# Optimization experiments

Hardware: AMD Instinct MI355X
Metric: run time of the kernel (lower is better)

The kernel has to match this reference:

```python
import jax, jax.numpy as jnp
import numpy as np

B, T, S, D, V = 8, 64, 512, 512, 50000


def setup_inputs() -> dict:
    key = jax.random.key(0)
    k1, k2, k3, k4, k5 = jax.random.split(key, 5)
    x = jax.random.normal(k1, (B, T, D), dtype=jnp.float32)
    attn_dist = jax.random.normal(k2, (B, T, S), dtype=jnp.float32)
    enc_batch_extend_vocab = jax.random.randint(k3, (B, S), 0, V, dtype=jnp.int64)
    W_proj = jax.random.normal(k4, (D, V), dtype=jnp.float32) * (1.0 / np.sqrt(D))
    b_proj = jnp.zeros((V,), dtype=jnp.float32)
    W_pgen = jax.random.normal(k5, (D, 1), dtype=jnp.float32) * (1.0 / np.sqrt(D))
    b_pgen = jnp.zeros((1,), dtype=jnp.float32)
    return {"x": x, "attn_dist": attn_dist,
            "enc_batch_extend_vocab": enc_batch_extend_vocab,
            "W_proj": W_proj, "b_proj": b_proj,
            "W_pgen": W_pgen, "b_pgen": b_pgen}


def reference(x, attn_dist, enc_batch_extend_vocab, W_proj, b_proj, W_pgen, b_pgen):
    # pointer-generator head, temp=1, beam_search=False
    temp = 1.0
    # p_gen gate: [B, T, 1]
    alpha = jax.nn.sigmoid(jnp.einsum('btd,de->bte', x, W_pgen) + b_pgen)
    # vocab projection + softmax: [B, T, V]
    logit = jnp.einsum('btd,dv->btv', x, W_proj) + b_proj
    vocab_dist = jax.nn.softmax(logit / temp, axis=2)
    vocab_dist_ = alpha * vocab_dist
    # copy distribution over source positions: [B, T, S]
    attn = jax.nn.softmax(attn_dist / temp, axis=-1)
    attn_ = (1.0 - alpha) * attn
    # scatter_add copy probs into vocab dim (index broadcast over T)
    b_idx = jnp.arange(B)[:, None, None]        # [B,1,1]
    t_idx = jnp.arange(T)[None, :, None]        # [1,T,1]
    v_idx = enc_batch_extend_vocab[:, None, :]  # [B,1,S]
    merged = vocab_dist_.at[b_idx, t_idx, v_idx].add(attn_)
    return jnp.log(merged)
```

## Files before the change

### kernel.cpp

```cpp
#include <hip/hip_runtime.h>
#include <math.h>
#include <stdint.h>

#define B_ 8
#define T_ 64
#define S_ 512
#define D_ 512
#define V_ 50000
#define VP_ 50176
#define M_ (B_*T_)
#define ROWB_ ((size_t)V_ * 4)

typedef __bf16 bf16_t;
typedef bf16_t bf16x8 __attribute__((ext_vector_type(8)));
typedef float  f32x4  __attribute__((ext_vector_type(4)));

__device__ inline float blk_sum(float v, float* sm) {
    #pragma unroll
    for (int o = 32; o > 0; o >>= 1) v += __shfl_down(v, o);
    int lane = threadIdx.x & 63, wid = threadIdx.x >> 6;
    __syncthreads();
    if (lane == 0) sm[wid] = v;
    __syncthreads();
    return sm[0] + sm[1] + sm[2] + sm[3];
}

__device__ inline float blk_max(float v, float* sm) {
    #pragma unroll
    for (int o = 32; o > 0; o >>= 1) v = fmaxf(v, __shfl_down(v, o));
    int lane = threadIdx.x & 63, wid = threadIdx.x >> 6;
    __syncthreads();
    if (lane == 0) sm[wid] = v;
    __syncthreads();
    return fmaxf(fmaxf(sm[0], sm[1]), fmaxf(sm[2], sm[3]));
}

__device__ inline void unpack8(uint4 u, float f[8]) {
    uint32_t w0 = u.x, w1 = u.y, w2 = u.z, w3 = u.w;
    f[0] = __uint_as_float(w0 << 16); f[1] = __uint_as_float(w0 & 0xffff0000u);
    f[2] = __uint_as_float(w1 << 16); f[3] = __uint_as_float(w1 & 0xffff0000u);
    f[4] = __uint_as_float(w2 << 16); f[5] = __uint_as_float(w2 & 0xffff0000u);
    f[6] = __uint_as_float(w3 << 16); f[7] = __uint_as_float(w3 & 0xffff0000u);
}

#define CONVB_ (98 * 16)
#define LTP2_ 516

__global__ __launch_bounds__(256) void kprep(
    const float* __restrict__ W, bf16_t* __restrict__ Wt,
    const float* __restrict__ x, const float* __restrict__ attn_dist,
    const float* __restrict__ W_pgen, const float* __restrict__ b_pgen,
    float* __restrict__ logalpha_out, float* __restrict__ attn_out, bf16_t* __restrict__ xb,
    const int* __restrict__ idx, int* __restrict__ owner_g)
{
    __shared__ bf16_t lt[32 * LTP2_];
    int bid = blockIdx.x;
    int tid = threadIdx.x;

    if (bid < CONVB_) {
        int vt = bid >> 4;
        int kb = bid & 15;
        int v0 = vt * 512, k0 = kb * 32;

        #pragma unroll
        for (int p = 0; p < 16; p++) {
            int i = p * 256 + tid;
            int k = i >> 7;
            int c4 = i & 127;
            int v = c4 * 4;
            float4 val = make_float4(0.f, 0.f, 0.f, 0.f);
            if (v0 + v < V_)
                val = *reinterpret_cast<const float4*>(&W[(size_t)(k0 + k) * V_ + v0 + v]);
            union { bf16_t h[4]; uint2 u; } pk;
            pk.h[0] = (bf16_t)val.x; pk.h[1] = (bf16_t)val.y;
            pk.h[2] = (bf16_t)val.z; pk.h[3] = (bf16_t)val.w;
            *reinterpret_cast<uint2*>(&lt[k * LTP2_ + v]) = pk.u;
        }
        __syncthreads();

        #pragma unroll
        for (int p = 0; p < 8; p++) {
            int i = p * 256 + tid;
            int v = i >> 2;
            int q = i & 3;
            union { ushort h[8]; uint4 u; } pk;
            #pragma unroll
            for (int j = 0; j < 8; j++)
                pk.h[j] = *reinterpret_cast<const ushort*>(&lt[(q * 8 + j) * LTP2_ + v]);
            *reinterpret_cast<uint4*>(&Wt[(size_t)(v0 + v) * D_ + k0 + q * 8]) = pk.u;
        }
    } else if (bid < CONVB_ + M_) {
        float* sm = reinterpret_cast<float*>(lt);
        int row = bid - CONVB_;

        float2 xv = reinterpret_cast<const float2*>(x + (size_t)row * D_)[tid];
        float2 wv = reinterpret_cast<const float2*>(W_pgen)[tid];
        union { bf16_t h[2]; uint32_t u; } pk;
        pk.h[0] = (bf16_t)xv.x; pk.h[1] = (bf16_t)xv.y;
        reinterpret_cast<uint32_t*>(xb + (size_t)row * D_)[tid] = pk.u;

        float dot = blk_sum(xv.x * wv.x + xv.y * wv.y, sm);
        float alpha = 1.f / (1.f + expf(-(dot + b_pgen[0])));
        if (tid == 0) logalpha_out[row] = logf(alpha);

        float a0 = attn_dist[(size_t)row * S_ + tid];
        float a1 = attn_dist[(size_t)row * S_ + tid + 256];
        float mx = blk_max(fmaxf(a0, a1), sm);
        float e0 = expf(a0 - mx), e1 = expf(a1 - mx);
        float s = blk_sum(e0 + e1, sm);
        float scale = (1.f - alpha) / s;
        attn_out[(size_t)row * S_ + tid]       = e0 * scale;
        attn_out[(size_t)row * S_ + tid + 256] = e1 * scale;
    } else {
        int* ids = reinterpret_cast<int*>(lt);
        int b = bid - (CONVB_ + M_);
        for (int s = tid; s < S_; s += 256) ids[s] = idx[b * S_ + s];
        __syncthreads();
        for (int s = tid; s < S_; s += 256) {
            int v = ids[s], o = s;
            for (int s2 = 0; s2 < s; s2++) if (ids[s2] == v) { o = s2; break; }
            owner_g[b * S_ + s] = o;
        }
    }
}

#define GBM 128
#define GBN 128
#define GBK 32
#define NT2_ (D_/GBK)

__global__ __launch_bounds__(256) void k2_mfma(
    const bf16_t* __restrict__ A, const bf16_t* __restrict__ Wt,
    const float* __restrict__ bias, char* __restrict__ outB)
{
    __shared__ bf16_t As0[GBM][GBK], As1[GBM][GBK];
    __shared__ bf16_t Bs0[GBN][GBK], Bs1[GBN][GBK];
    int tid  = threadIdx.x;
    int lane = tid & 63;
    int w    = tid >> 6;
    int wm   = w >> 1, wn = w & 1;
    int bn = blockIdx.x * GBN;
    int bm = blockIdx.y * GBM;

    f32x4 acc[4][4] = {};

#define STAGE(dstA, dstB, k0)                                                          \
    {                                                                                  \
        _Pragma("unroll")                                                              \
        for (int i = 0; i < 2; i++) {                                                  \
            int e = (w * 2 + i) * 512 + lane * 8;                                      \
            int r = e >> 5, c = e & 31;                                                \
            __builtin_amdgcn_global_load_lds(                                          \
                (const __attribute__((address_space(1))) void*)                        \
                    &A[(size_t)(bm + r) * D_ + (k0) + c],                              \
                (__attribute__((address_space(3))) void*)&dstA[(w * 2 + i) * 16][0],   \
                16, 0, 0);                                                             \
            __builtin_amdgcn_global_load_lds(                                          \
                (const __attribute__((address_space(1))) void*)                        \
                    &Wt[(size_t)(bn + r) * D_ + (k0) + c],                             \
                (__attribute__((address_space(3))) void*)&dstB[(w * 2 + i) * 16][0],   \
                16, 0, 0);                                                             \
        }                                                                              \
    }

#define COMPUTE(srcA, srcB)                                                            \
    {                                                                                  \
        bf16x8 af[4], bfr[4];                                                          \
        int kb = (lane >> 4) * 8;                                                      \
        _Pragma("unroll")                                                              \
        for (int mi = 0; mi < 4; mi++)                                                 \
            af[mi] = *reinterpret_cast<const bf16x8*>(&srcA[wm * 64 + mi * 16 + (lane & 15)][kb]); \
        _Pragma("unroll")                                                              \
        for (int ni = 0; ni < 4; ni++)                                                 \
            bfr[ni] = *reinterpret_cast<const bf16x8*>(&srcB[wn * 64 + ni * 16 + (lane & 15)][kb]); \
        _Pragma("unroll")                                                              \
        for (int mi = 0; mi < 4; mi++)                                                 \
            _Pragma("unroll")                                                          \
            for (int ni = 0; ni < 4; ni++)                                             \
                acc[mi][ni] = __builtin_amdgcn_mfma_f32_16x16x32_bf16(af[mi], bfr[ni], acc[mi][ni], 0, 0, 0); \
    }

    STAGE(As0, Bs0, 0);
    asm volatile("s_waitcnt vmcnt(0)" ::: "memory");
    __syncthreads();

    #pragma unroll
    for (int tt = 0; tt < NT2_ / 2; tt++) {
        int k0 = tt * 2 * GBK;
        if (k0 + GBK < D_) STAGE(As1, Bs1, k0 + GBK);
        COMPUTE(As0, Bs0);
        asm volatile("s_waitcnt vmcnt(0)" ::: "memory");
        __syncthreads();
        if (k0 + 2 * GBK < D_) STAGE(As0, Bs0, k0 + 2 * GBK);
        COMPUTE(As1, Bs1);
        asm volatile("s_waitcnt vmcnt(0)" ::: "memory");
        __syncthreads();
    }
#undef STAGE
#undef COMPUTE

    int cm = bm + wm * 64, cn = bn + wn * 64;
    #pragma unroll
    for (int ni = 0; ni < 4; ni++) {
        int n = cn + ni * 16 + (lane & 15);
        float bv = (n < V_) ? bias[n] : 0.f;
        #pragma unroll
        for (int mi = 0; mi < 4; mi++) {
            int rbase = cm + mi * 16 + (lane >> 4) * 4;
            #pragma unroll
            for (int r = 0; r < 4; r++) {
                bf16_t val = (bf16_t)(acc[mi][ni][r] + bv);
                *reinterpret_cast<bf16_t*>(outB + (size_t)(rbase + r) * ROWB_ + 2 * (size_t)n) = val;
            }
        }
    }
}

#define CHUNK_ 2048
#define NCH_ ((V_ + CHUNK_ - 1) / CHUNK_)

__global__ __launch_bounds__(256) void k345_final(
    char* __restrict__ outB, const float* __restrict__ attn_, const int* __restrict__ idx,
    const int* __restrict__ owner_g, const float* __restrict__ logalpha)
{
    __shared__ float att[S_];
    __shared__ int own[S_], ids[S_];
    __shared__ float smm[4], sms[4];
    int row = blockIdx.x;
    int b = row >> 6;
    int tid = threadIdx.x;
    int lane = tid & 63, wid = tid >> 6;

    for (int s = tid; s < S_; s += 256) {
        att[s] = attn_[(size_t)row * S_ + s];
        own[s] = owner_g[b * S_ + s];
        ids[s] = idx[b * S_ + s];
    }

    const uint4* L4 = reinterpret_cast<const uint4*>(outB + (size_t)row * ROWB_);
    float m = -INFINITY, se = 0.f;
    for (int i = tid; i < V_ / 8; i += 256) {
        uint4 u = L4[i];
        float f[8]; unpack8(u, f);
        float m8 = fmaxf(fmaxf(fmaxf(f[0], f[1]), fmaxf(f[2], f[3])),
                         fmaxf(fmaxf(f[4], f[5]), fmaxf(f[6], f[7])));
        float mn = fmaxf(m, m8);
        se = se * __expf(m - mn)
           + __expf(f[0] - mn) + __expf(f[1] - mn) + __expf(f[2] - mn) + __expf(f[3] - mn)
           + __expf(f[4] - mn) + __expf(f[5] - mn) + __expf(f[6] - mn) + __expf(f[7] - mn);
        m = mn;
    }
    #pragma unroll
    for (int o = 32; o > 0; o >>= 1) {
        float m2 = __shfl_down(m, o);
        float s2 = __shfl_down(se, o);
        float mn = fmaxf(m, m2);
        if (mn == -INFINITY) { se = 0.f; }
        else se = se * __expf(m - mn) + s2 * __expf(m2 - mn);
        m = mn;
    }
    __syncthreads();
    if (lane == 0) { smm[wid] = m; sms[wid] = se; }
    __syncthreads();
    float M = smm[0], Ssum = sms[0];
    #pragma unroll
    for (int wv = 1; wv < 4; wv++) {
        float m2 = smm[wv], s2 = sms[wv];
        float mn = fmaxf(M, m2);
        if (mn != -INFINITY) Ssum = Ssum * __expf(M - mn) + s2 * __expf(m2 - mn);
        M = mn;
    }
    float logden = M + logf(Ssum);
    float c_ = logalpha[row] - logden;

    for (int s = tid; s < S_; s += 256)
        if (own[s] != s) atomicAdd(&att[own[s]], att[s]);
    __syncthreads();

    const ushort* Lrow = reinterpret_cast<const ushort*>(outB + (size_t)row * ROWB_);
    float* frow = reinterpret_cast<float*>(outB + (size_t)row * ROWB_);
    for (int c = NCH_ - 1; c >= 0; c--) {
        int i0 = c * CHUNK_ + tid * 8;
        uint4 u = make_uint4(0, 0, 0, 0);
        bool act = (i0 + 8 <= V_);
        if (act) u = *reinterpret_cast<const uint4*>(Lrow + i0);
        __syncthreads();
        if (act) {
            float f[8]; unpack8(u, f);
            float4 lo = make_float4(f[0] + c_, f[1] + c_, f[2] + c_, f[3] + c_);
            float4 hi = make_float4(f[4] + c_, f[5] + c_, f[6] + c_, f[7] + c_);
            *reinterpret_cast<float4*>(frow + i0)     = lo;
            *reinterpret_cast<float4*>(frow + i0 + 4) = hi;
        }
        __syncthreads();
    }

    for (int s = tid; s < S_; s += 256) {
        if (own[s] == s) {
            int v = ids[s];
            frow[v] = logf(expf(frow[v]) + att[s]);
        }
    }
}

__global__ __launch_bounds__(256) void k1_alpha_attn(
    const float* __restrict__ x, const float* __restrict__ attn_dist,
    const float* __restrict__ W_pgen, const float* __restrict__ b_pgen,
    float* __restrict__ logalpha_out, float* __restrict__ attn_out)
{
    __shared__ float sm[4];
    int row = blockIdx.x;
    int tid = threadIdx.x;
    float2 xv = reinterpret_cast<const float2*>(x + (size_t)row * D_)[tid];
    float2 wv = reinterpret_cast<const float2*>(W_pgen)[tid];
    float dot = blk_sum(xv.x * wv.x + xv.y * wv.y, sm);
    float alpha = 1.f / (1.f + expf(-(dot + b_pgen[0])));
    if (tid == 0) logalpha_out[row] = logf(alpha);
    float a0 = attn_dist[(size_t)row * S_ + tid];
    float a1 = attn_dist[(size_t)row * S_ + tid + 256];
    float mx = blk_max(fmaxf(a0, a1), sm);
    float e0 = expf(a0 - mx), e1 = expf(a1 - mx);
    float s = blk_sum(e0 + e1, sm);
    float scale = (1.f - alpha) / s;
    attn_out[(size_t)row * S_ + tid]       = e0 * scale;
    attn_out[(size_t)row * S_ + tid + 256] = e1 * scale;
}

__global__ __launch_bounds__(512) void k5a_owner(const int* __restrict__ idx, int* __restrict__ owner_g)
{
    __shared__ int ids[S_];
    int b = blockIdx.x;
    int s = threadIdx.x;
    ids[s] = idx[b * S_ + s];
    __syncthreads();
    int v = ids[s], o = s;
    for (int s2 = 0; s2 < s; s2++) if (ids[s2] == v) { o = s2; break; }
    owner_g[b * S_ + s] = o;
}

#define BM 64
#define BN 64
#define BK 16
__global__ __launch_bounds__(256) void k2_gemm(
    const float* __restrict__ A, const float* __restrict__ W,
    const float* __restrict__ bias, float* __restrict__ C)
{
    __shared__ float As2[BK][BM + 1];
    __shared__ float Bs2[BK][BN + 1];
    int bn = blockIdx.x * BN;
    int bm = blockIdx.y * BM;
    int tid = threadIdx.x;
    int tx = tid & 15;
    int ty = tid >> 4;
    bool full_n = (bn + BN <= V_);
    float acc[4][4] = {};
    for (int k0 = 0; k0 < D_; k0 += BK) {
        {
            int i = tid * 4;
            int row = i >> 4, col = i & 15;
            const float4 av = *reinterpret_cast<const float4*>(&A[(size_t)(bm + row) * D_ + k0 + col]);
            As2[col + 0][row] = av.x; As2[col + 1][row] = av.y;
            As2[col + 2][row] = av.z; As2[col + 3][row] = av.w;
        }
        {
            int i = tid * 4;
            int row = i >> 6, col = i & 63;
            int gn = bn + col;
            if (full_n) {
                const float4 bv = *reinterpret_cast<const float4*>(&W[(size_t)(k0 + row) * V_ + gn]);
                Bs2[row][col + 0] = bv.x; Bs2[row][col + 1] = bv.y;
                Bs2[row][col + 2] = bv.z; Bs2[row][col + 3] = bv.w;
            } else {
                #pragma unroll
                for (int j = 0; j < 4; j++)
                    Bs2[row][col + j] = (gn + j < V_) ? W[(size_t)(k0 + row) * V_ + gn + j] : 0.f;
            }
        }
        __syncthreads();
        #pragma unroll
        for (int kk = 0; kk < BK; kk++) {
            float a[4], b[4];
            #pragma unroll
            for (int i = 0; i < 4; i++) a[i] = As2[kk][ty * 4 + i];
            #pragma unroll
            for (int j = 0; j < 4; j++) b[j] = Bs2[kk][tx + j * 16];
            #pragma unroll
            for (int i = 0; i < 4; i++)
                #pragma unroll
                for (int j = 0; j < 4; j++)
                    acc[i][j] += a[i] * b[j];
        }
        __syncthreads();
    }
    #pragma unroll
    for (int i = 0; i < 4; i++) {
        int m = bm + ty * 4 + i;
        #pragma unroll
        for (int j = 0; j < 4; j++) {
            int n = bn + tx + j * 16;
            if (n < V_) C[(size_t)m * V_ + n] = acc[i][j] + bias[n];
        }
    }
}

__global__ __launch_bounds__(256) void k3_stats(const float* __restrict__ C, float* __restrict__ logden)
{
    __shared__ float smm[4], sms[4];
    int row = blockIdx.x;
    const float4* p = reinterpret_cast<const float4*>(C + (size_t)row * V_);
    float m = -INFINITY, s = 0.f;
    for (int i = threadIdx.x; i < V_ / 4; i += 256) {
        float4 v = p[i];
        float m4 = fmaxf(fmaxf(v.x, v.y), fmaxf(v.z, v.w));
        if (m4 > m) { s *= expf(m - m4); m = m4; }
        s += expf(v.x - m) + expf(v.y - m) + expf(v.z - m) + expf(v.w - m);
    }
    #pragma unroll
    for (int o = 32; o > 0; o >>= 1) {
        float m2 = __shfl_down(m, o);
        float s2 = __shfl_down(s, o);
        float mn = fmaxf(m, m2);
        s = s * expf(m - mn) + s2 * expf(m2 - mn);
        m = mn;
    }
    int lane = threadIdx.x & 63, wid = threadIdx.x >> 6;
    if (lane == 0) { smm[wid] = m; sms[wid] = s; }
    __syncthreads();
    if (threadIdx.x == 0) {
        float M = smm[0], S = sms[0];
        #pragma unroll
        for (int wv = 1; wv < 4; wv++) {
            float m2 = smm[wv], s2 = sms[wv];
            float mn = fmaxf(M, m2);
            S = S * expf(M - mn) + s2 * expf(m2 - mn);
            M = mn;
        }
        logden[row] = M + logf(S);
    }
}

__global__ __launch_bounds__(256) void k4_scale(
    float* __restrict__ C, const float* __restrict__ logalpha, const float* __restrict__ logden)
{
    int row = blockIdx.y;
    int i = blockIdx.x * 256 + threadIdx.x;
    if (i >= V_ / 4) return;
    float c_ = logalpha[row] - logden[row];
    float4* p = reinterpret_cast<float4*>(C + (size_t)row * V_) + i;
    float4 v = *p;
    v.x += c_; v.y += c_; v.z += c_; v.w += c_;
    *p = v;
}

__global__ __launch_bounds__(256) void k5_scatter_log(
    float* __restrict__ C, const float* __restrict__ attn_, const int* __restrict__ idx,
    const int* __restrict__ owner_g)
{
    __shared__ float att[S_];
    __shared__ int own[S_], ids[S_];
    int row = blockIdx.x;
    int b = row >> 6;
    int tid = threadIdx.x;
    for (int s = tid; s < S_; s += 256) {
        att[s] = attn_[(size_t)row * S_ + s];
        own[s] = owner_g[b * S_ + s];
        ids[s] = idx[b * S_ + s];
    }
    __syncthreads();
    for (int s = tid; s < S_; s += 256)
        if (own[s] != s) atomicAdd(&att[own[s]], att[s]);
    __syncthreads();
    for (int s = tid; s < S_; s += 256) {
        if (own[s] == s) {
            int v = ids[s];
            float* p = &C[(size_t)row * V_ + v];
            *p = logf(expf(*p) + att[s]);
        }
    }
}

extern "C" void kernel_launch(void* const* d_in, const int* in_sizes, int n_in,
                              void* d_out, int out_size, void* d_ws, size_t ws_size,
                              hipStream_t stream) {
    const float* x         = (const float*)d_in[0];
    const float* attn_dist = (const float*)d_in[1];
    const int*   ebev      = (const int*)  d_in[2];
    const float* W_proj    = (const float*)d_in[3];
    const float* b_proj    = (const float*)d_in[4];
    const float* W_pgen    = (const float*)d_in[5];
    const float* b_pgen    = (const float*)d_in[6];
    float* out = (float*)d_out;
    char*  outB = (char*)d_out;

    float*  logalpha = (float*)d_ws;
    float*  logden   = logalpha + M_;
    float*  attn_    = logden + M_;
    int*    owner    = (int*)(attn_ + (size_t)B_ * T_ * S_);
    bf16_t* xb       = (bf16_t*)(owner + (size_t)B_ * S_);
    bf16_t* Wt       = xb + (size_t)M_ * D_;
    size_t need = (size_t)(2 * M_ + B_ * T_ * S_ + B_ * S_) * 4
                + (size_t)M_ * D_ * 2 + (size_t)VP_ * D_ * 2;

    if (ws_size >= need) {
        kprep<<<CONVB_ + M_ + B_, 256, 0, stream>>>(
            W_proj, Wt, x, attn_dist, W_pgen, b_pgen, logalpha, attn_, xb, ebev, owner);

        dim3 g2(VP_ / GBN, M_ / GBM);
        k2_mfma<<<g2, 256, 0, stream>>>(xb, Wt, b_proj, outB);

        k345_final<<<M_, 256, 0, stream>>>(outB, attn_, ebev, owner, logalpha);
    } else {
        k1_alpha_attn<<<M_, 256, 0, stream>>>(x, attn_dist, W_pgen, b_pgen, logalpha, attn_);
        k5a_owner<<<B_, 512, 0, stream>>>(ebev, owner);
        dim3 g2((V_ + BN - 1) / BN, M_ / BM);
        k2_gemm<<<g2, 256, 0, stream>>>(x, W_proj, b_proj, out);
        k3_stats<<<M_, 256, 0, stream>>>(out, logden);
        dim3 g4((V_ / 4 + 255) / 256, M_);
        k4_scale<<<g4, 256, 0, stream>>>(out, logalpha, logden);
        k5_scatter_log<<<M_, 256, 0, stream>>>(out, attn_, ebev, owner);
    }
}
```

Measured before the change: 154.3 us.

## Retile weight transpose to full-K 64-column tiles with XOR-swizzled LDS

Restructures the fp32-to-bf16 transpose of W_proj in the prep kernel. Each block now handles 64 vocab columns across all 512 K rows instead of a 512x32 tile. Elements are written into shared memory with an XOR swizzle, so each output row is read back as contiguous 16-byte chunks and written to Wt as full 1KB rows. This removes the 8 scalar 2-byte LDS gathers per output vector and the short 64-byte global write segments. The cost is fewer, larger blocks using more shared memory (about 66KB), plus scalar 2-byte LDS stores in the load phase.

Result: slower. 159.7 us (+3.5%).

```diff
diff --git a/kernel.cpp b/kernel.cpp
--- a/kernel.cpp
+++ b/kernel.cpp
@@ -43,8 +43,8 @@
     f[6] = __uint_as_float(w3 << 16); f[7] = __uint_as_float(w3 & 0xffff0000u);
 }
 
-#define CONVB_ (98 * 16)
-#define LTP2_ 516
+#define TRB_ 784
+#define LTK_ 520
 
 __global__ __launch_bounds__(256) void kprep(
     const float* __restrict__ W, bf16_t* __restrict__ Wt,
@@ -53,45 +53,41 @@
     float* __restrict__ logalpha_out, float* __restrict__ attn_out, bf16_t* __restrict__ xb,
     const int* __restrict__ idx, int* __restrict__ owner_g)
 {
-    __shared__ bf16_t lt[32 * LTP2_];
+    __shared__ bf16_t lt[64 * LTK_];
     int bid = blockIdx.x;
     int tid = threadIdx.x;
 
-    if (bid < CONVB_) {
-        int vt = bid >> 4;
-        int kb = bid & 15;
-        int v0 = vt * 512, k0 = kb * 32;
-
-        #pragma unroll
+    if (bid < TRB_) {
+        int v0 = bid * 64;
+        #pragma unroll 4
+        for (int p = 0; p < 32; p++) {
+            int i = p * 256 + tid;
+            int k = i >> 4;
+            int v = (i & 15) * 4;
+            int gv = v0 + v;
+            float4 val = make_float4(0.f, 0.f, 0.f, 0.f);
+            if (gv < V_)
+                val = *reinterpret_cast<const float4*>(&W[(size_t)k * V_ + gv]);
+            const float* vf = reinterpret_cast<const float*>(&val);
+            #pragma unroll
+            for (int j = 0; j < 4; j++) {
+                int vv = v + j;
+                lt[vv * LTK_ + (k ^ ((vv & 7) << 3))] = (bf16_t)vf[j];
+            }
+        }
+        __syncthreads();
+        #pragma unroll 4
         for (int p = 0; p < 16; p++) {
             int i = p * 256 + tid;
-            int k = i >> 7;
-            int c4 = i & 127;
-            int v = c4 * 4;
-            float4 val = make_float4(0.f, 0.f, 0.f, 0.f);
-            if (v0 + v < V_)
-                val = *reinterpret_cast<const float4*>(&W[(size_t)(k0 + k) * V_ + v0 + v]);
-            union { bf16_t h[4]; uint2 u; } pk;
-            pk.h[0] = (bf16_t)val.x; pk.h[1] = (bf16_t)val.y;
-            pk.h[2] = (bf16_t)val.z; pk.h[3] = (bf16_t)val.w;
-            *reinterpret_cast<uint2*>(&lt[k * LTP2_ + v]) = pk.u;
-        }
-        __syncthreads();
-
-        #pragma unroll
-        for (int p = 0; p < 8; p++) {
-            int i = p * 256 + tid;
-            int v = i >> 2;
-            int q = i & 3;
-            union { ushort h[8]; uint4 u; } pk;
-            #pragma unroll
-            for (int j = 0; j < 8; j++)
-                pk.h[j] = *reinterpret_cast<const ushort*>(&lt[(q * 8 + j) * LTP2_ + v]);
-            *reinterpret_cast<uint4*>(&Wt[(size_t)(v0 + v) * D_ + k0 + q * 8]) = pk.u;
-        }
-    } else if (bid < CONVB_ + M_) {
+            int vv = i >> 6;
+            int kc8 = (i & 63) * 8;
+            uint4 u = *reinterpret_cast<const uint4*>(
+                &lt[vv * LTK_ + (kc8 ^ ((vv & 7) << 3))]);
+            *reinterpret_cast<uint4*>(&Wt[(size_t)(v0 + vv) * D_ + kc8]) = u;
+        }
+    } else if (bid < TRB_ + M_) {
         float* sm = reinterpret_cast<float*>(lt);
-        int row = bid - CONVB_;
+        int row = bid - TRB_;
 
         float2 xv = reinterpret_cast<const float2*>(x + (size_t)row * D_)[tid];
         float2 wv = reinterpret_cast<const float2*>(W_pgen)[tid];
@@ -113,7 +109,7 @@
         attn_out[(size_t)row * S_ + tid + 256] = e1 * scale;
     } else {
         int* ids = reinterpret_cast<int*>(lt);
-        int b = bid - (CONVB_ + M_);
+        int b = bid - (TRB_ + M_);
         for (int s = tid; s < S_; s += 256) ids[s] = idx[b * S_ + s];
         __syncthreads();
         for (int s = tid; s < S_; s += 256) {
@@ -502,7 +498,7 @@
                 + (size_t)M_ * D_ * 2 + (size_t)VP_ * D_ * 2;
 
     if (ws_size >= need) {
-        kprep<<<CONVB_ + M_ + B_, 256, 0, stream>>>(
+        kprep<<<TRB_ + M_ + B_, 256, 0, stream>>>(
             W_proj, Wt, x, attn_dist, W_pgen, b_pgen, logalpha, attn_, xb, ebev, owner);
 
         dim3 g2(VP_ / GBN, M_ / GBM);
```
